# Kernel optimization log

Measured on AMD Instinct MI355X. Metric: run time of the kernel, lower is better.

## Reference

```python
import jax, jax.numpy as jnp
import numpy as np

LAMBDA_A = 1.0
NUM_ITER = 3
K = 64
BN_EPS = 1e-5


def setup_inputs() -> dict:
    key = jax.random.key(0)
    ks = jax.random.split(key, 8)
    B, C, H, W = 16, 512, 64, 64
    x = jax.random.normal(ks[0], (B, C, H, W), dtype=jnp.float32)
    # codebook mu: init normal(std~sqrt(2/k)) then L2-normalize along dim=1 (k axis), as in torch init
    mu = jax.random.normal(ks[1], (C, K), dtype=jnp.float32) * np.sqrt(2.0 / K)
    mu = mu / jnp.maximum(jnp.linalg.norm(mu, axis=1, keepdims=True), 1e-12)
    # 1x1 convs expressed as (out, in) matrices
    stem_w = jax.random.normal(ks[2], (C, C), dtype=jnp.float32) * np.sqrt(2.0 / C)
    stem_b = jnp.zeros((C,), dtype=jnp.float32)
    head_w = jax.random.normal(ks[3], (C, C), dtype=jnp.float32) * np.sqrt(2.0 / C)
    head_b = jnp.zeros((C,), dtype=jnp.float32)
    bn_gamma = jnp.ones((C,), dtype=jnp.float32)
    bn_beta = jnp.zeros((C,), dtype=jnp.float32)
    return {"x": x, "mu": mu, "stem_w": stem_w, "stem_b": stem_b,
            "head_w": head_w, "head_b": head_b,
            "bn_gamma": bn_gamma, "bn_beta": bn_beta}


def _conv1x1(x, w, b):
    # x: (B,C,H,W), w: (O,C)
    return jnp.einsum('bchw,oc->bohw', x, w) + b[None, :, None, None]


def reference(x, mu, stem_w, stem_b, head_w, head_b, bn_gamma, bn_beta):
    B, C, H, W = x.shape
    N = H * W
    y = _conv1x1(x, stem_w, stem_b)                 # (B,C,H,W)
    yf = y.reshape(B, C, N).transpose(0, 2, 1)      # (B,N,C)

    mu_b = jnp.broadcast_to(mu[None], (B, C, K))    # (B,C,K)
    z = None
    for _ in range(NUM_ITER):
        z = jax.nn.softmax(LAMBDA_A * jnp.einsum('bnc,bck->bnk', yf, mu_b), axis=2)
        zn = z / (1e-6 + z.sum(axis=1, keepdims=True))
        mu_b = jnp.einsum('bnc,bnk->bck', yf, zn)
        mu_b = mu_b / jnp.maximum(jnp.linalg.norm(mu_b, axis=1, keepdims=True), 1e-12)

    # EM loop runs under no_grad in torch
    mu_b = jax.lax.stop_gradient(mu_b)
    z = jax.lax.stop_gradient(z)

    y2 = jnp.einsum('bck,bnk->bcn', mu_b, z).reshape(B, C, H, W)

    # head: ReLU -> 1x1 conv -> BatchNorm2d (training-mode batch stats)
    h = _conv1x1(jnp.maximum(y2, 0.0), head_w, head_b)
    mean = h.mean(axis=(0, 2, 3), keepdims=True)
    var = h.var(axis=(0, 2, 3), keepdims=True)
    h = (h - mean) * jax.lax.rsqrt(var + BN_EPS)
    h = h * bn_gamma[None, :, None, None] + bn_beta[None, :, None, None]

    return jnp.maximum(h + x, 0.0)
```

## Files before the change

### kernel.cpp

```cpp
#include <hip/hip_runtime.h>


typedef _Float16 half_t;
typedef _Float16 half8 __attribute__((ext_vector_type(8)));
typedef float f32x4 __attribute__((ext_vector_type(4)));

#define GLD_LDS(gp, lp) __builtin_amdgcn_global_load_lds( \
    (const __attribute__((address_space(1))) void*)(gp),  \
    (__attribute__((address_space(3))) void*)(lp), 16, 0, 0)

constexpr int CB = 16;
constexpr int CC = 512;
constexpr int CN = 4096;
constexpr int CKK = 64;
constexpr long MALL = (long)CB * CN;

__global__ __launch_bounds__(256) void prep(
    const float* __restrict__ stem_w, const float* __restrict__ head_w,
    const float* __restrict__ mu,
    half_t* __restrict__ swh, half_t* __restrict__ hwh,
    half_t* __restrict__ muT, half_t* __restrict__ muck)
{
  int i = blockIdx.x * 256 + threadIdx.x;
  swh[i] = (half_t)stem_w[i];
  hwh[i] = (half_t)head_w[i];
  if (i < CC * CKK) {
    int c = i >> 6, k = i & 63;
    half_t v = (half_t)mu[i];
    for (int b = 0; b < CB; ++b) {
      muT[(long)b * CKK * CC + (long)k * CC + c] = v;
      muck[(long)b * CC * CKK + i] = v;
    }
  }
}

template <typename Tin>
__global__ __launch_bounds__(256) void transpose2(
    const Tin* __restrict__ in, half_t* __restrict__ out, int R, int S)
{
  __shared__ half_t t[64][65];
  const int s0 = blockIdx.x * 64, r0 = blockIdx.y * 64;
  const long bz = blockIdx.z;
  const Tin* ib = in + bz * (long)R * S;
  half_t* ob = out + bz * (long)R * S;
  const int tid = threadIdx.x;
  const int cl = tid & 63, rw = tid >> 6;
#pragma unroll
  for (int it = 0; it < 16; ++it) {
    int r = it * 4 + rw;
    t[cl][r] = (half_t)(float)ib[(long)(r0 + r) * S + s0 + cl];
  }
  __syncthreads();
#pragma unroll
  for (int it = 0; it < 16; ++it) {
    int s = it * 4 + rw;
    ob[(long)(s0 + s) * R + r0 + cl] = t[s][cl];
  }
}

template <int BM, int BN, int MODE>
__global__ __launch_bounds__(256) void gemm_abt(
    const half_t* __restrict__ A, const half_t* __restrict__ Bm,
    half_t* __restrict__ Co, float* __restrict__ Cacc,
    const float* __restrict__ bias,
    int M, int Nn, int Kk, int ksplit, long sA, long sB, long sC)
{
  constexpr int FM = BM / 32, FN = BN / 32;
  __shared__ __align__(16) half_t lA[BM * 64];
  __shared__ __align__(16) half_t lB[BN * 64];
  const int tid = threadIdx.x, wid = tid >> 6, lane = tid & 63;
  const int tilesN = Nn / BN;
  const int tm = blockIdx.x / tilesN, tn = blockIdx.x % tilesN;
  const long bz = blockIdx.z;
  const half_t* Ab = A + bz * sA + (long)tm * BM * Kk;
  const half_t* Bb = Bm + bz * sB + (long)tn * BN * Kk;
  const int ksteps = Kk >> 6;
  const int per = ksteps / ksplit;
  const int ks0 = blockIdx.y * per, ks1 = ks0 + per;
  const int wr = wid >> 1, wc = wid & 1;

  f32x4 acc[FM][FN];
#pragma unroll
  for (int i = 0; i < FM; ++i)
#pragma unroll
    for (int j = 0; j < FN; ++j) acc[i][j] = f32x4{0.f, 0.f, 0.f, 0.f};

  for (int ks = ks0; ks < ks1; ++ks) {
    __syncthreads();
    {
      const half_t* ga = Ab + (long)ks * 64;
#pragma unroll
      for (int c = wid; c < BM / 8; c += 4) {
        const half_t* g = ga + (long)(c * 8 + (lane >> 3)) * Kk + (lane & 7) * 8;
        GLD_LDS(g, &lA[c * 512]);
      }
      const half_t* gb = Bb + (long)ks * 64;
#pragma unroll
      for (int c = wid; c < BN / 8; c += 4) {
        const half_t* g = gb + (long)(c * 8 + (lane >> 3)) * Kk + (lane & 7) * 8;
        GLD_LDS(g, &lB[c * 512]);
      }
    }
    __syncthreads();
#pragma unroll
    for (int kk = 0; kk < 2; ++kk) {
      half8 af[FM], bfr[FN];
#pragma unroll
      for (int i = 0; i < FM; ++i)
        af[i] = *(const half8*)&lA[(wr * (BM / 2) + i * 16 + (lane & 15)) * 64 +
                                   kk * 32 + (lane >> 4) * 8];
#pragma unroll
      for (int j = 0; j < FN; ++j)
        bfr[j] = *(const half8*)&lB[(wc * (BN / 2) + j * 16 + (lane & 15)) * 64 +
                                    kk * 32 + (lane >> 4) * 8];
#pragma unroll
      for (int i = 0; i < FM; ++i)
#pragma unroll
        for (int j = 0; j < FN; ++j)
          acc[i][j] = __builtin_amdgcn_mfma_f32_16x16x32_f16(af[i], bfr[j],
                                                             acc[i][j], 0, 0, 0);
    }
  }

#pragma unroll
  for (int j = 0; j < FN; ++j) {
    const int n = tn * BN + wc * (BN / 2) + j * 16 + (lane & 15);
    float bv = 0.f;
    if constexpr (MODE & 1) bv = bias[n];
#pragma unroll
    for (int i = 0; i < FM; ++i) {
      const int mbase = tm * BM + wr * (BM / 2) + i * 16 + ((lane >> 4) << 2);
#pragma unroll
      for (int r = 0; r < 4; ++r) {
        const long idx = bz * sC + (long)(mbase + r) * Nn + n;
        if constexpr ((MODE & 4) != 0) {
          atomicAdd(&Cacc[idx], acc[i][j][r]);
        } else {
          float v = acc[i][j][r] + bv;
          if constexpr ((MODE & 2) != 0) v = fmaxf(v, 0.f);
          Co[idx] = (half_t)v;
        }
      }
    }
  }
}

__global__ __launch_bounds__(256) void s_softmax(
    const half_t* __restrict__ Yf, const half_t* __restrict__ muT,
    half_t* __restrict__ z, half_t* __restrict__ zT)
{
  __shared__ __align__(16) union {
    struct { half_t a[128 * 64]; half_t b[64 * 64]; } st;
    struct { float s[128 * 65]; half_t zh[128 * 68]; } p2;
  } sm;
  const int tid = threadIdx.x, wid = tid >> 6, lane = tid & 63;
  const int tm = blockIdx.x;
  const long bz = blockIdx.z;
  const half_t* Ab = Yf + bz * (long)CN * CC + (long)tm * 128 * CC;
  const half_t* Bb = muT + bz * (long)CKK * CC;
  const int wr = wid >> 1, wc = wid & 1;

  f32x4 acc[4][2];
#pragma unroll
  for (int i = 0; i < 4; ++i)
#pragma unroll
    for (int j = 0; j < 2; ++j) acc[i][j] = f32x4{0.f, 0.f, 0.f, 0.f};

  for (int ks = 0; ks < 8; ++ks) {
    __syncthreads();
    {
      const half_t* ga = Ab + (long)ks * 64;
#pragma unroll
      for (int c = wid; c < 16; c += 4) {
        const half_t* g = ga + (long)(c * 8 + (lane >> 3)) * CC + (lane & 7) * 8;
        GLD_LDS(g, &sm.st.a[c * 512]);
      }
      const half_t* gb = Bb + (long)ks * 64;
#pragma unroll
      for (int c = wid; c < 8; c += 4) {
        const half_t* g = gb + (long)(c * 8 + (lane >> 3)) * CC + (lane & 7) * 8;
        GLD_LDS(g, &sm.st.b[c * 512]);
      }
    }
    __syncthreads();
#pragma unroll
    for (int kk = 0; kk < 2; ++kk) {
      half8 af[4], bfr[2];
#pragma unroll
      for (int i = 0; i < 4; ++i)
        af[i] = *(const half8*)&sm.st.a[(wr * 64 + i * 16 + (lane & 15)) * 64 +
                                        kk * 32 + (lane >> 4) * 8];
#pragma unroll
      for (int j = 0; j < 2; ++j)
        bfr[j] = *(const half8*)&sm.st.b[(wc * 32 + j * 16 + (lane & 15)) * 64 +
                                         kk * 32 + (lane >> 4) * 8];
#pragma unroll
      for (int i = 0; i < 4; ++i)
#pragma unroll
        for (int j = 0; j < 2; ++j)
          acc[i][j] = __builtin_amdgcn_mfma_f32_16x16x32_f16(af[i], bfr[j],
                                                             acc[i][j], 0, 0, 0);
    }
  }
  __syncthreads();
#pragma unroll
  for (int j = 0; j < 2; ++j)
#pragma unroll
    for (int i = 0; i < 4; ++i)
#pragma unroll
      for (int r = 0; r < 4; ++r) {
        int nl = wc * 32 + j * 16 + (lane & 15);
        int ml = wr * 64 + i * 16 + ((lane >> 4) << 2) + r;
        sm.p2.s[ml * 65 + nl] = acc[i][j][r];
      }
  __syncthreads();
  if (tid < 128) {
    float row[64];
    float mx = -1e30f;
#pragma unroll
    for (int k = 0; k < 64; ++k) { row[k] = sm.p2.s[tid * 65 + k]; mx = fmaxf(mx, row[k]); }
    float sum = 0.f;
#pragma unroll
    for (int k = 0; k < 64; ++k) { row[k] = __expf(row[k] - mx); sum += row[k]; }
    const float inv = 1.f / sum;
#pragma unroll
    for (int k = 0; k < 64; ++k) sm.p2.zh[tid * 68 + k] = (half_t)(row[k] * inv);
  }
  __syncthreads();
  {
    const int nl = tid >> 1, seg = tid & 1;
    const long base = bz * (long)CN * CKK + (long)(tm * 128 + nl) * CKK + seg * 32;
#pragma unroll
    for (int g = 0; g < 4; ++g) {
      half8 v;
#pragma unroll
      for (int e = 0; e < 8; ++e) v[e] = sm.p2.zh[nl * 68 + seg * 32 + g * 8 + e];
      *(half8*)&z[base + g * 8] = v;
    }
  }
  {
    const int k = tid >> 2, seg = tid & 3;
    const long base = bz * (long)CKK * CN + (long)k * CN + tm * 128 + seg * 32;
#pragma unroll
    for (int g = 0; g < 4; ++g) {
      half8 v;
#pragma unroll
      for (int e = 0; e < 8; ++e) v[e] = sm.p2.zh[(seg * 32 + g * 8 + e) * 68 + k];
      *(half8*)&zT[base + g * 8] = v;
    }
  }
}

__global__ __launch_bounds__(64) void mu_norm(
    const float* __restrict__ acc, half_t* __restrict__ muT, half_t* __restrict__ muck)
{
  const int bk = blockIdx.x;
  const int b = bk >> 6, k = bk & 63;
  const float* row = acc + (long)bk * CC;
  const int t = threadIdx.x;
  float v[8]; float s = 0.f;
#pragma unroll
  for (int e = 0; e < 8; ++e) { v[e] = row[t * 8 + e]; s += v[e] * v[e]; }
#pragma unroll
  for (int m = 1; m < 64; m <<= 1) s += __shfl_xor(s, m);
  const float inv = 1.f / fmaxf(sqrtf(s), 1e-12f);
  half8 o;
#pragma unroll
  for (int e = 0; e < 8; ++e) o[e] = (half_t)(v[e] * inv);
  *(half8*)&muT[(long)bk * CC + t * 8] = o;
  half_t* mc = muck + (long)b * CC * CKK;
#pragma unroll
  for (int e = 0; e < 8; ++e) mc[(long)(t * 8 + e) * CKK + k] = o[e];
}

__global__ __launch_bounds__(512) void bn_stats(
    const half_t* __restrict__ hf, float* __restrict__ stats)
{
  const int c = threadIdx.x;
  const long r0 = (long)blockIdx.x * 256;
  float s = 0.f, s2 = 0.f;
  for (int i = 0; i < 256; ++i) {
    float v = (float)hf[(r0 + i) * CC + c];
    s += v; s2 += v * v;
  }
  atomicAdd(&stats[c], s);
  atomicAdd(&stats[CC + c], s2);
}

__global__ void bn_param(const float* __restrict__ stats,
                         const float* __restrict__ gamma, const float* __restrict__ beta,
                         float* __restrict__ scsh)
{
  const int c = threadIdx.x;
  const float cnt = 1.f / 65536.f;
  const float mean = stats[c] * cnt;
  const float var = stats[CC + c] * cnt - mean * mean;
  const float sc = gamma[c] * rsqrtf(var + 1e-5f);
  scsh[c] = sc;
  scsh[CC + c] = beta[c] - mean * sc;
}

__global__ __launch_bounds__(256) void bn_final(
    const half_t* __restrict__ hf, const float* __restrict__ x,
    const float* __restrict__ scale, const float* __restrict__ shift,
    float* __restrict__ out)
{
  __shared__ float t[64][65];
  const int n0 = blockIdx.x * 64, c0 = blockIdx.y * 64;
  const long bz = blockIdx.z;
  const half_t* hb = hf + bz * (long)CN * CC;
  const int tid = threadIdx.x, cl = tid & 63, rw = tid >> 6;
#pragma unroll
  for (int it = 0; it < 16; ++it) {
    int n = it * 4 + rw;
    t[cl][n] = (float)hb[(long)(n0 + n) * CC + c0 + cl];
  }
  __syncthreads();
  const float* xb = x + bz * (long)CC * CN;
  float* ob = out + bz * (long)CC * CN;
#pragma unroll
  for (int it = 0; it < 16; ++it) {
    int c = it * 4 + rw;
    const float sc = scale[c0 + c], sh = shift[c0 + c];
    const long idx = (long)(c0 + c) * CN + n0 + cl;
    float v = t[c][cl] * sc + sh + xb[idx];
    ob[idx] = fmaxf(v, 0.f);
  }
}

extern "C" void kernel_launch(void* const* d_in, const int* in_sizes, int n_in,
                              void* d_out, int out_size, void* d_ws, size_t ws_size,
                              hipStream_t stream)
{
  const float* x      = (const float*)d_in[0];
  const float* mu     = (const float*)d_in[1];
  const float* stem_w = (const float*)d_in[2];
  const float* stem_b = (const float*)d_in[3];
  const float* head_w = (const float*)d_in[4];
  const float* head_b = (const float*)d_in[5];
  const float* bn_g   = (const float*)d_in[6];
  const float* bn_b   = (const float*)d_in[7];
  float* out = (float*)d_out;

  const size_t NEED = 214ull << 20;
  if (ws_size < NEED) {
    hipMemsetAsync(d_out, 0, (size_t)out_size * 4, stream);
    return;
  }
  char* ws = (char*)d_ws;
  const long MB = 1 << 20;
  half_t* xT   = (half_t*)(ws);
  half_t* Yf   = (half_t*)(ws + 64 * MB);
  half_t* ycn  = (half_t*)(ws + 128 * MB);
  half_t* z    = (half_t*)(ws + 192 * MB);
  half_t* zT   = (half_t*)(ws + 200 * MB);
  half_t* muT  = (half_t*)(ws + 208 * MB);
  half_t* muck = (half_t*)(ws + 209 * MB);
  float* muacc = (float*)(ws + 210 * MB);
  half_t* swh  = (half_t*)(ws + 212 * MB);
  half_t* hwh  = (half_t*)(ws + 212 * MB + 512 * 1024);
  float* stats = (float*)(ws + 213 * MB);
  float* scsh  = (float*)(ws + 213 * MB + 8 * 1024);
  half_t* y2f = xT;
  half_t* hf  = ycn;

  prep<<<1024, 256, 0, stream>>>(stem_w, head_w, mu, swh, hwh, muT, muck);
  transpose2<float><<<dim3(64, 8, 16), 256, 0, stream>>>(x, xT, CC, CN);
  gemm_abt<128, 128, 1><<<dim3(2048, 1, 1), 256, 0, stream>>>(
      xT, swh, Yf, nullptr, stem_b, (int)MALL, CC, CC, 1, 0, 0, 0);
  transpose2<half_t><<<dim3(8, 64, 16), 256, 0, stream>>>(Yf, ycn, CN, CC);

  for (int it = 0; it < 3; ++it) {
    s_softmax<<<dim3(32, 1, 16), 256, 0, stream>>>(Yf, muT, z, zT);
    hipMemsetAsync(muacc, 0, (size_t)CB * CKK * CC * 4, stream);
    gemm_abt<64, 128, 4><<<dim3(4, 4, 16), 256, 0, stream>>>(
        zT, ycn, nullptr, muacc, nullptr, CKK, CC, CN, 4,
        (long)CKK * CN, (long)CC * CN, (long)CKK * CC);
    mu_norm<<<CB * CKK, 64, 0, stream>>>(muacc, muT, muck);
  }
  gemm_abt<128, 128, 2><<<dim3(128, 1, 16), 256, 0, stream>>>(
      z, muck, y2f, nullptr, nullptr, CN, CC, CKK, 1,
      (long)CN * CKK, (long)CC * CKK, (long)CN * CC);
  gemm_abt<128, 128, 1><<<dim3(2048, 1, 1), 256, 0, stream>>>(
      y2f, hwh, hf, nullptr, head_b, (int)MALL, CC, CC, 1, 0, 0, 0);

  hipMemsetAsync(stats, 0, 2 * CC * 4, stream);
  bn_stats<<<256, 512, 0, stream>>>(hf, stats);
  bn_param<<<1, 512, 0, stream>>>(stats, bn_g, bn_b, scsh);
  bn_final<<<dim3(64, 8, 16), 256, 0, stream>>>(hf, x, scsh, scsh + CC, out);
}
```

Measured before the change: 440.3 us.

## Fuse transposes into GEMM epilogues via LDS and restructure BN stats/final

The stem GEMM now writes both the row-major and the channel-major outputs through an LDS-staged epilogue, which removes the separate fp16 transpose kernel. The head GEMM writes its output directly in channel-major layout. That lets BN stats run one block per channel with vectorized reads and no atomics or memset, and lets the BN final pass run as a flat vectorized elementwise kernel with no transpose. The GEMMs also get an 8-way block-index swizzle for L2 locality, and s_softmax skips writing z except on the last iteration. In exchange the epilogues need extra shared memory, add strided LDS reads, and the 128x128 epilogue path is hardcoded.

New measurement: 441.6 us. Within noise of the previous version (+0.3%).

```diff
diff --git a/kernel.cpp b/kernel.cpp
--- a/kernel.cpp
+++ b/kernel.cpp
@@ -2,6 +2,7 @@
 
 
 typedef _Float16 half_t;
+typedef _Float16 half4 __attribute__((ext_vector_type(4)));
 typedef _Float16 half8 __attribute__((ext_vector_type(8)));
 typedef float f32x4 __attribute__((ext_vector_type(4)));
 
@@ -14,6 +15,10 @@
 constexpr int CN = 4096;
 constexpr int CKK = 64;
 constexpr long MALL = (long)CB * CN;
+
+__device__ inline int swz8(int bid, int n) {
+  return (bid & 7) * (n >> 3) + (bid >> 3);
+}
 
 __global__ __launch_bounds__(256) void prep(
     const float* __restrict__ stem_w, const float* __restrict__ head_w,
@@ -34,43 +39,48 @@
   }
 }
 
-template <typename Tin>
-__global__ __launch_bounds__(256) void transpose2(
-    const Tin* __restrict__ in, half_t* __restrict__ out, int R, int S)
+__global__ __launch_bounds__(256) void xpose(
+    const float* __restrict__ in, half_t* __restrict__ outT)
 {
   __shared__ half_t t[64][65];
   const int s0 = blockIdx.x * 64, r0 = blockIdx.y * 64;
   const long bz = blockIdx.z;
-  const Tin* ib = in + bz * (long)R * S;
-  half_t* ob = out + bz * (long)R * S;
-  const int tid = threadIdx.x;
-  const int cl = tid & 63, rw = tid >> 6;
+  const float* ib = in + bz * (long)CC * CN;
+  half_t* ob = outT + bz * (long)CC * CN;
+  const int tid = threadIdx.x, cl = tid & 63, rw = tid >> 6;
 #pragma unroll
   for (int it = 0; it < 16; ++it) {
     int r = it * 4 + rw;
-    t[cl][r] = (half_t)(float)ib[(long)(r0 + r) * S + s0 + cl];
+    t[cl][r] = (half_t)ib[(long)(r0 + r) * CN + s0 + cl];
   }
   __syncthreads();
 #pragma unroll
   for (int it = 0; it < 16; ++it) {
     int s = it * 4 + rw;
-    ob[(long)(s0 + s) * R + r0 + cl] = t[s][cl];
-  }
-}
-
-template <int BM, int BN, int MODE>
+    ob[(long)(s0 + s) * CC + r0 + cl] = t[s][cl];
+  }
+}
+
+template <int BM, int BN, int MODE, int EPI, bool SWZ>
 __global__ __launch_bounds__(256) void gemm_abt(
     const half_t* __restrict__ A, const half_t* __restrict__ Bm,
-    half_t* __restrict__ Co, float* __restrict__ Cacc,
-    const float* __restrict__ bias,
+    half_t* __restrict__ Co, half_t* __restrict__ CoT,
+    float* __restrict__ Cacc, const float* __restrict__ bias,
     int M, int Nn, int Kk, int ksplit, long sA, long sB, long sC)
 {
   constexpr int FM = BM / 32, FN = BN / 32;
-  __shared__ __align__(16) half_t lA[BM * 64];
-  __shared__ __align__(16) half_t lB[BN * 64];
+  constexpr int STG = (BM + BN) * 64;
+  constexpr int EPS = (EPI != 0) ? BN * (BM + 4) : 0;
+  constexpr int TOT = STG > EPS ? STG : EPS;
+  __shared__ __align__(16) half_t smem[TOT];
+  half_t* lA = smem;
+  half_t* lB = smem + BM * 64;
+
   const int tid = threadIdx.x, wid = tid >> 6, lane = tid & 63;
+  int bid = blockIdx.x;
+  if constexpr (SWZ) bid = swz8(bid, gridDim.x);
   const int tilesN = Nn / BN;
-  const int tm = blockIdx.x / tilesN, tn = blockIdx.x % tilesN;
+  const int tm = bid / tilesN, tn = bid % tilesN;
   const long bz = blockIdx.z;
   const half_t* Ab = A + bz * sA + (long)tm * BM * Kk;
   const half_t* Bb = Bm + bz * sB + (long)tn * BN * Kk;
@@ -122,23 +132,72 @@
     }
   }
 
-#pragma unroll
-  for (int j = 0; j < FN; ++j) {
-    const int n = tn * BN + wc * (BN / 2) + j * 16 + (lane & 15);
-    float bv = 0.f;
-    if constexpr (MODE & 1) bv = bias[n];
-#pragma unroll
-    for (int i = 0; i < FM; ++i) {
-      const int mbase = tm * BM + wr * (BM / 2) + i * 16 + ((lane >> 4) << 2);
-#pragma unroll
-      for (int r = 0; r < 4; ++r) {
-        const long idx = bz * sC + (long)(mbase + r) * Nn + n;
-        if constexpr ((MODE & 4) != 0) {
-          atomicAdd(&Cacc[idx], acc[i][j][r]);
-        } else {
+  if constexpr (EPI != 0) {
+    static_assert(BM == 128 && BN == 128, "LDS epilogue assumes 128x128");
+    constexpr int PIT = BM + 4;
+    half_t* ep = smem;
+    __syncthreads();
+#pragma unroll
+    for (int j = 0; j < FN; ++j) {
+      const int nl = wc * 64 + j * 16 + (lane & 15);
+      float bv = 0.f;
+      if constexpr (MODE & 1) bv = bias[tn * BN + nl];
+#pragma unroll
+      for (int i = 0; i < FM; ++i) {
+        const int ml = wr * 64 + i * 16 + ((lane >> 4) << 2);
+        half4 h;
+#pragma unroll
+        for (int r = 0; r < 4; ++r) {
           float v = acc[i][j][r] + bv;
-          if constexpr ((MODE & 2) != 0) v = fmaxf(v, 0.f);
-          Co[idx] = (half_t)v;
+          if constexpr (MODE & 2) v = fmaxf(v, 0.f);
+          h[r] = (half_t)v;
+        }
+        *(half4*)&ep[nl * PIT + ml] = h;
+      }
+    }
+    __syncthreads();
+    const long rowbase = (long)tm * BM;
+    if constexpr (EPI & 1) {
+#pragma unroll
+      for (int s = 0; s < 8; ++s) {
+        const int q = tid + 256 * s;
+        const int m = q & 127, cc = q >> 7;
+        half8 v;
+#pragma unroll
+        for (int e = 0; e < 8; ++e) v[e] = ep[(cc * 8 + e) * PIT + m];
+        *(half8*)&Co[bz * sC + (rowbase + m) * Nn + tn * BN + cc * 8] = v;
+      }
+    }
+    if constexpr (EPI & 2) {
+#pragma unroll
+      for (int s = 0; s < 8; ++s) {
+        const int q = tid + 256 * s;
+        const int cl = q & 127, mc = q >> 7;
+        half8 v = *(const half8*)&ep[cl * PIT + mc * 8];
+        const long row = rowbase + mc * 8;
+        const long b = row >> 12, nsp = row & 4095;
+        *(half8*)&CoT[(b * Nn + tn * BN + cl) * 4096 + nsp] = v;
+      }
+    }
+  } else {
+#pragma unroll
+    for (int j = 0; j < FN; ++j) {
+      const int n = tn * BN + wc * (BN / 2) + j * 16 + (lane & 15);
+      float bv = 0.f;
+      if constexpr (MODE & 1) bv = bias[n];
+#pragma unroll
+      for (int i = 0; i < FM; ++i) {
+        const int mbase = tm * BM + wr * (BM / 2) + i * 16 + ((lane >> 4) << 2);
+#pragma unroll
+        for (int r = 0; r < 4; ++r) {
+          const long idx = bz * sC + (long)(mbase + r) * Nn + n;
+          if constexpr ((MODE & 4) != 0) {
+            atomicAdd(&Cacc[idx], acc[i][j][r]);
+          } else {
+            float v = acc[i][j][r] + bv;
+            if constexpr ((MODE & 2) != 0) v = fmaxf(v, 0.f);
+            Co[idx] = (half_t)v;
+          }
         }
       }
     }
@@ -147,7 +206,7 @@
 
 __global__ __launch_bounds__(256) void s_softmax(
     const half_t* __restrict__ Yf, const half_t* __restrict__ muT,
-    half_t* __restrict__ z, half_t* __restrict__ zT)
+    half_t* __restrict__ zp, half_t* __restrict__ zT)
 {
   __shared__ __align__(16) union {
     struct { half_t a[128 * 64]; half_t b[64 * 64]; } st;
@@ -227,7 +286,7 @@
     for (int k = 0; k < 64; ++k) sm.p2.zh[tid * 68 + k] = (half_t)(row[k] * inv);
   }
   __syncthreads();
-  {
+  if (zp) {
     const int nl = tid >> 1, seg = tid & 1;
     const long base = bz * (long)CN * CKK + (long)(tm * 128 + nl) * CKK + seg * 32;
 #pragma unroll
@@ -235,7 +294,7 @@
       half8 v;
 #pragma unroll
       for (int e = 0; e < 8; ++e) v[e] = sm.p2.zh[nl * 68 + seg * 32 + g * 8 + e];
-      *(half8*)&z[base + g * 8] = v;
+      *(half8*)&zp[base + g * 8] = v;
     }
   }
   {
@@ -273,18 +332,29 @@
   for (int e = 0; e < 8; ++e) mc[(long)(t * 8 + e) * CKK + k] = o[e];
 }
 
-__global__ __launch_bounds__(512) void bn_stats(
-    const half_t* __restrict__ hf, float* __restrict__ stats)
-{
-  const int c = threadIdx.x;
-  const long r0 = (long)blockIdx.x * 256;
+__global__ __launch_bounds__(256) void bn_stats2(
+    const half_t* __restrict__ hcn, float* __restrict__ stats)
+{
+  const int c = blockIdx.x, tid = threadIdx.x;
   float s = 0.f, s2 = 0.f;
-  for (int i = 0; i < 256; ++i) {
-    float v = (float)hf[(r0 + i) * CC + c];
-    s += v; s2 += v * v;
-  }
-  atomicAdd(&stats[c], s);
-  atomicAdd(&stats[CC + c], s2);
+  for (int b = 0; b < CB; ++b) {
+    const half_t* p = hcn + ((long)b * CC + c) * CN;
+    for (int i = tid * 8; i < CN; i += 2048) {
+      half8 v = *(const half8*)&p[i];
+#pragma unroll
+      for (int e = 0; e < 8; ++e) { float f = (float)v[e]; s += f; s2 += f * f; }
+    }
+  }
+#pragma unroll
+  for (int m = 1; m < 64; m <<= 1) { s += __shfl_xor(s, m); s2 += __shfl_xor(s2, m); }
+  __shared__ float r[8];
+  const int wid = tid >> 6;
+  if ((tid & 63) == 0) { r[wid] = s; r[4 + wid] = s2; }
+  __syncthreads();
+  if (tid == 0) {
+    stats[c] = r[0] + r[1] + r[2] + r[3];
+    stats[CC + c] = r[4] + r[5] + r[6] + r[7];
+  }
 }
 
 __global__ void bn_param(const float* __restrict__ stats,
@@ -300,32 +370,23 @@
   scsh[CC + c] = beta[c] - mean * sc;
 }
 
-__global__ __launch_bounds__(256) void bn_final(
-    const half_t* __restrict__ hf, const float* __restrict__ x,
-    const float* __restrict__ scale, const float* __restrict__ shift,
-    float* __restrict__ out)
-{
-  __shared__ float t[64][65];
-  const int n0 = blockIdx.x * 64, c0 = blockIdx.y * 64;
-  const long bz = blockIdx.z;
-  const half_t* hb = hf + bz * (long)CN * CC;
-  const int tid = threadIdx.x, cl = tid & 63, rw = tid >> 6;
-#pragma unroll
-  for (int it = 0; it < 16; ++it) {
-    int n = it * 4 + rw;
-    t[cl][n] = (float)hb[(long)(n0 + n) * CC + c0 + cl];
-  }
-  __syncthreads();
-  const float* xb = x + bz * (long)CC * CN;
-  float* ob = out + bz * (long)CC * CN;
-#pragma unroll
-  for (int it = 0; it < 16; ++it) {
-    int c = it * 4 + rw;
-    const float sc = scale[c0 + c], sh = shift[c0 + c];
-    const long idx = (long)(c0 + c) * CN + n0 + cl;
-    float v = t[c][cl] * sc + sh + xb[idx];
-    ob[idx] = fmaxf(v, 0.f);
-  }
+__global__ __launch_bounds__(256) void bn_final2(
+    const half_t* __restrict__ hcn, const float* __restrict__ x,
+    const float* __restrict__ scsh, float* __restrict__ out)
+{
+  const long i8 = (long)blockIdx.x * 256 + threadIdx.x;
+  const int c = (int)((i8 >> 9) & 511);
+  const float sc = scsh[c], sh = scsh[CC + c];
+  half8 h = *(const half8*)&hcn[i8 * 8];
+  f32x4 x0 = *(const f32x4*)&x[i8 * 8];
+  f32x4 x1 = *(const f32x4*)&x[i8 * 8 + 4];
+  f32x4 o0, o1;
+#pragma unroll
+  for (int e = 0; e < 4; ++e) o0[e] = fmaxf((float)h[e] * sc + sh + x0[e], 0.f);
+#pragma unroll
+  for (int e = 0; e < 4; ++e) o1[e] = fmaxf((float)h[4 + e] * sc + sh + x1[e], 0.f);
+  *(f32x4*)&out[i8 * 8] = o0;
+  *(f32x4*)&out[i8 * 8 + 4] = o1;
 }
 
 extern "C" void kernel_launch(void* const* d_in, const int* in_sizes, int n_in,
@@ -362,30 +423,29 @@
   float* stats = (float*)(ws + 213 * MB);
   float* scsh  = (float*)(ws + 213 * MB + 8 * 1024);
   half_t* y2f = xT;
-  half_t* hf  = ycn;
+  half_t* hcn = Yf;
 
   prep<<<1024, 256, 0, stream>>>(stem_w, head_w, mu, swh, hwh, muT, muck);
-  transpose2<float><<<dim3(64, 8, 16), 256, 0, stream>>>(x, xT, CC, CN);
-  gemm_abt<128, 128, 1><<<dim3(2048, 1, 1), 256, 0, stream>>>(
-      xT, swh, Yf, nullptr, stem_b, (int)MALL, CC, CC, 1, 0, 0, 0);
-  transpose2<half_t><<<dim3(8, 64, 16), 256, 0, stream>>>(Yf, ycn, CN, CC);
+  xpose<<<dim3(64, 8, 16), 256, 0, stream>>>(x, xT);
+  gemm_abt<128, 128, 1, 3, true><<<dim3(2048, 1, 1), 256, 0, stream>>>(
+      xT, swh, Yf, ycn, nullptr, stem_b, (int)MALL, CC, CC, 1, 0, 0, 0);
 
   for (int it = 0; it < 3; ++it) {
-    s_softmax<<<dim3(32, 1, 16), 256, 0, stream>>>(Yf, muT, z, zT);
+    s_softmax<<<dim3(32, 1, 16), 256, 0, stream>>>(
+        Yf, muT, (it == 2) ? z : nullptr, zT);
     hipMemsetAsync(muacc, 0, (size_t)CB * CKK * CC * 4, stream);
-    gemm_abt<64, 128, 4><<<dim3(4, 4, 16), 256, 0, stream>>>(
-        zT, ycn, nullptr, muacc, nullptr, CKK, CC, CN, 4,
+    gemm_abt<64, 128, 4, 0, false><<<dim3(4, 4, 16), 256, 0, stream>>>(
+        zT, ycn, nullptr, nullptr, muacc, nullptr, CKK, CC, CN, 4,
         (long)CKK * CN, (long)CC * CN, (long)CKK * CC);
     mu_norm<<<CB * CKK, 64, 0, stream>>>(muacc, muT, muck);
   }
-  gemm_abt<128, 128, 2><<<dim3(128, 1, 16), 256, 0, stream>>>(
-      z, muck, y2f, nullptr, nullptr, CN, CC, CKK, 1,
+  gemm_abt<128, 128, 2, 1, true><<<dim3(128, 1, 16), 256, 0, stream>>>(
+      z, muck, y2f, nullptr, nullptr, nullptr, CN, CC, CKK, 1,
       (long)CN * CKK, (long)CC * CKK, (long)CN * CC);
-  gemm_abt<128, 128, 1><<<dim3(2048, 1, 1), 256, 0, stream>>>(
-      y2f, hwh, hf, nullptr, head_b, (int)MALL, CC, CC, 1, 0, 0, 0);
-
-  hipMemsetAsync(stats, 0, 2 * CC * 4, stream);
-  bn_stats<<<256, 512, 0, stream>>>(hf, stats);
+  gemm_abt<128, 128, 1, 2, true><<<dim3(2048, 1, 1), 256, 0, stream>>>(
+      y2f, hwh, nullptr, hcn, nullptr, head_b, (int)MALL, CC, CC, 1, 0, 0, 0);
+
+  bn_stats2<<<CC, 256, 0, stream>>>(hcn, stats);
   bn_param<<<1, 512, 0, stream>>>(stats, bn_g, bn_b, scsh);
-  bn_final<<<dim3(64, 8, 16), 256, 0, stream>>>(hf, x, scsh, scsh + CC, out);
-}
+  bn_final2<<<16384, 256, 0, stream>>>(hcn, x, scsh, out);
+}
```
